# Kernel tuning notes

Hardware: AMD Instinct MI355X
Metric: run time of the kernel (lower is better)

## Reference

```python
import jax, jax.numpy as jnp
import numpy as np

N_PAIRS = 1_600_000   # total neighbor pairs (len(idx_i))
N_ATOMS = 50_000      # number of distinct center atoms (avg 32 neighbors each)


def setup_inputs() -> dict:
    key = jax.random.key(0)
    # sorted center indices -> consecutive ragged segments, like a neighbor list
    idx_i = jnp.sort(jax.random.randint(key, (N_PAIRS,), 0, N_ATOMS, dtype=jnp.int32))
    return {"idx_i": idx_i}


def reference(idx_i):
    # NOTE: output shape is data-dependent (sum_i C(c_i,2)), so this runs eagerly
    # (the concrete sizes below are python ints pulled from the input values),
    # exactly mirroring torch.unique_consecutive + per-segment torch.combinations.
    n = idx_i.shape[0]
    # --- unique_consecutive(return_counts=True), vectorized ---
    change = jnp.concatenate([jnp.ones((1,), bool), idx_i[1:] != idx_i[:-1]])
    seg_id = jnp.cumsum(change.astype(jnp.int32)) - 1          # [n] segment id per pair
    n_seg = int(seg_id[-1]) + 1
    counts = jnp.bincount(seg_id, length=n_seg)                 # [n_seg] c_i
    seg_off = jnp.concatenate([jnp.zeros((1,), counts.dtype), jnp.cumsum(counts)[:-1]])
    # --- per-segment number of unordered pairs C(c,2) ---
    tri_counts = counts * (counts - 1) // 2
    tri_off = jnp.concatenate([jnp.zeros((1,), tri_counts.dtype), jnp.cumsum(tri_counts)[:-1]])
    T = int(jnp.sum(tri_counts))
    # --- one flat vectorized pass over all T triples ---
    idx_i_triples = jnp.repeat(jnp.arange(n_seg, dtype=jnp.int32), tri_counts,
                               total_repeat_length=T)           # [T] segment index
    r = jnp.arange(T, dtype=counts.dtype) - tri_off[idx_i_triples]  # local triple rank
    c = counts[idx_i_triples]                                   # segment size per triple
    M = c * (c - 1) // 2
    rr = M - 1 - r                                              # rank counted from the end
    # triangular-root decode of condensed upper-triangle index (c is small -> fp32 exact)
    a_rev = jnp.floor((jnp.sqrt(8.0 * rr.astype(jnp.float32) + 1.0) - 1.0) / 2.0).astype(c.dtype)
    a = c - 2 - a_rev                                           # first local neighbor pos
    b = c - 1 - (rr - a_rev * (a_rev + 1) // 2)                 # second local neighbor pos (> a)
    base = seg_off[idx_i_triples]
    idx_j_triples = base + a
    idx_k_triples = base + b
    return (idx_i_triples, idx_j_triples, idx_k_triples)
```

## Files before the change

### kernel.cpp

```cpp
#include <hip/hip_runtime.h>

#define THREADS 256
#define EPT 8
#define FILL_BLOCKS 4096

__device__ __forceinline__ int blockReduceSum(int v, int* sdata) {
    int tid = threadIdx.x;
    sdata[tid] = v;
    __syncthreads();
    for (int off = THREADS >> 1; off > 0; off >>= 1) {
        if (tid < off) sdata[tid] += sdata[tid + off];
        __syncthreads();
    }
    int r = sdata[0];
    __syncthreads();
    return r;
}

__device__ __forceinline__ int blockScanIncl(int v, int* sdata) {
    int tid = threadIdx.x;
    sdata[tid] = v;
    __syncthreads();
    for (int off = 1; off < THREADS; off <<= 1) {
        int t = 0;
        if (tid >= off) t = sdata[tid - off];
        __syncthreads();
        if (tid >= off) sdata[tid] += t;
        __syncthreads();
    }
    int r = sdata[tid];
    __syncthreads();
    return r;
}

__device__ __forceinline__ int blockExclScanMax(int v, int* sdata) {
    int tid = threadIdx.x;
    sdata[tid] = v;
    __syncthreads();
    for (int off = 1; off < THREADS; off <<= 1) {
        int t = -1;
        if (tid >= off) t = sdata[tid - off];
        __syncthreads();
        if (tid >= off) sdata[tid] = max(sdata[tid], t);
        __syncthreads();
    }
    int r = (tid == 0) ? -1 : sdata[tid - 1];
    __syncthreads();
    return r;
}

__device__ int findPrevStart(const int* __restrict__ idx, int B0,
                             int* sdata, int* s_found) {
    int tid = threadIdx.x;
    if (tid == 0) *s_found = -1;
    __syncthreads();
    int res = -1;
    for (int step = 0; res < 0; ++step) {
        int p = B0 - 1 - step * THREADS - tid;
        int cand = -1;
        if (p >= 0) {
            bool f = (p == 0) || (idx[p - 1] != idx[p]);
            if (f) cand = p;
        }
        sdata[tid] = cand;
        __syncthreads();
        for (int off = THREADS >> 1; off > 0; off >>= 1) {
            if (tid < off) sdata[tid] = max(sdata[tid], sdata[tid + off]);
            __syncthreads();
        }
        if (tid == 0 && sdata[0] >= 0) *s_found = sdata[0];
        __syncthreads();
        res = *s_found;
        __syncthreads();
    }
    return res;
}

__global__ void k_chunkstats(const int* __restrict__ idx, int n,
                             int* __restrict__ chunkCnt,
                             int* __restrict__ chunkTriSum) {
    __shared__ int sdata[THREADS];
    __shared__ int s_tmp;
    int tid = threadIdx.x, bid = blockIdx.x;
    int B0 = bid * (THREADS * EPT);

    int prevStart = 0;
    if (bid > 0) prevStart = findPrevStart(idx, B0, sdata, &s_tmp);

    int base = B0 + tid * EPT;
    int cnt = 0, myLast = -1;
    for (int j = 0; j < EPT; ++j) {
        int p = base + j;
        if (p < n) {
            bool f = (p == 0) || (idx[p - 1] != idx[p]);
            if (f) { ++cnt; myLast = p; }
        }
    }
    int before = blockExclScanMax(myLast, sdata);
    int lastStart = max(prevStart, before);
    int sumq = 0;
    for (int j = 0; j < EPT; ++j) {
        int p = base + j;
        if (p < n) {
            if ((p == 0) || (idx[p - 1] != idx[p])) lastStart = p;
            sumq += p - lastStart;
        }
    }
    int c = blockReduceSum(cnt, sdata);
    int q = blockReduceSum(sumq, sdata);
    if (tid == 0) { chunkCnt[bid] = c; chunkTriSum[bid] = q; }
}

__global__ void k_emit(const int* __restrict__ idx, int n, int NB,
                       const int* __restrict__ chunkCnt,
                       const int* __restrict__ chunkTriSum,
                       int* __restrict__ segOff, int* __restrict__ triOff,
                       int* __restrict__ nsegPtr) {
    __shared__ int sdata[THREADS];
    __shared__ int s_tmp;
    int tid = threadIdx.x, bid = blockIdx.x;
    int B0 = bid * (THREADS * EPT);

    int prevStart = 0;
    if (bid > 0) prevStart = findPrevStart(idx, B0, sdata, &s_tmp);

    int pv = 0, tv = 0;
    for (int i = tid; i < bid; i += THREADS) {
        pv += chunkCnt[i];
        tv += chunkTriSum[i];
    }
    int segBase = blockReduceSum(pv, sdata);
    int triBase = blockReduceSum(tv, sdata);

    int base = B0 + tid * EPT;
    int cnt = 0, myLast = -1;
    for (int j = 0; j < EPT; ++j) {
        int p = base + j;
        if (p < n) {
            bool f = (p == 0) || (idx[p - 1] != idx[p]);
            if (f) { ++cnt; myLast = p; }
        }
    }
    int before = blockExclScanMax(myLast, sdata);
    int lastStart0 = max(prevStart, before);

    int lastStart = lastStart0;
    int sumq = 0;
    for (int j = 0; j < EPT; ++j) {
        int p = base + j;
        if (p < n) {
            if ((p == 0) || (idx[p - 1] != idx[p])) lastStart = p;
            sumq += p - lastStart;
        }
    }

    int inclC = blockScanIncl(cnt, sdata);
    int inclQ = blockScanIncl(sumq, sdata);
    int ord  = segBase + inclC - cnt;
    int tcur = triBase + inclQ - sumq;

    lastStart = lastStart0;
    for (int j = 0; j < EPT; ++j) {
        int p = base + j;
        if (p < n) {
            bool f = (p == 0) || (idx[p - 1] != idx[p]);
            if (f) {
                segOff[ord] = p;
                triOff[ord] = tcur;
                ++ord;
                lastStart = p;
            }
            tcur += p - lastStart;
        }
    }
    if (bid == NB - 1 && tid == THREADS - 1) {
        int nseg = segBase + inclC;
        *nsegPtr = nseg;
        segOff[nseg] = n;
    }
}

__device__ __forceinline__ void decodeRank(int rr, int c, int& a, int& b) {
    int k = (int)floorf((sqrtf((float)(8 * rr + 1)) - 1.0f) * 0.5f);
    if (k < 0) k = 0;
    while ((k + 1) * (k + 2) / 2 <= rr) ++k;
    while (k * (k + 1) / 2 > rr) --k;
    a = c - 2 - k;
    b = c - 1 - (rr - k * (k + 1) / 2);
}

__device__ __forceinline__ void emitOne(int r, int M, int c, int t0, int baseP,
                                        int s, int* __restrict__ outI,
                                        int* __restrict__ outJ,
                                        int* __restrict__ outK) {
    int a, b;
    decodeRank(M - 1 - r, c, a, b);
    int t = t0 + r;
    outI[t] = s;
    outJ[t] = baseP + a;
    outK[t] = baseP + b;
}

template <int PH>
__device__ __forceinline__ void storeQuad(int* __restrict__ P, int t, int4 v) {
    if constexpr (PH == 0) {
        *reinterpret_cast<int4*>(P + t) = v;
    } else if constexpr (PH == 2) {
        *reinterpret_cast<int2*>(P + t)     = make_int2(v.x, v.y);
        *reinterpret_cast<int2*>(P + t + 2) = make_int2(v.z, v.w);
    } else {
        P[t] = v.x;
        *reinterpret_cast<int2*>(P + t + 1) = make_int2(v.y, v.z);
        P[t + 3] = v.w;
    }
}

template <int TMOD4>
__global__ void k_fill(const int* __restrict__ segOff,
                       const int* __restrict__ triOff,
                       const int* __restrict__ nsegPtr, int T,
                       int* __restrict__ outI, int* __restrict__ outJ,
                       int* __restrict__ outK) {
    constexpr int PHJ = TMOD4 & 3;
    constexpr int PHK = (2 * TMOD4) & 3;
    int nseg = *nsegPtr;
    int w = blockIdx.x * (THREADS / 64) + (threadIdx.x >> 6);
    int lane = threadIdx.x & 63;
    int nW = gridDim.x * (THREADS / 64);
    long long tlo = (long long)T * w / nW;
    long long thi = (long long)T * (w + 1) / nW;
    if (tlo >= thi) return;

    int lo = 0, hi = nseg - 1;
    while (lo < hi) {
        int mid = (lo + hi + 1) >> 1;
        if (triOff[mid] <= (int)tlo) lo = mid; else hi = mid - 1;
    }
    int s = lo;
    long long t = tlo;
    while (t < thi && s < nseg) {
        int baseP = segOff[s];
        int c = segOff[s + 1] - baseP;
        int M = c * (c - 1) / 2;
        int t0 = triOff[s];
        int rstart = (int)(t - t0);
        int rend = M;
        { long long cap = thi - t0; if (cap < (long long)rend) rend = (int)cap; }

        int rA = rstart + ((4 - ((t0 + rstart) & 3)) & 3);
        if (rA > rend) rA = rend;
        int rB = rA + ((rend - rA) & ~3);

        for (int r = rstart + lane; r < rA; r += 64)
            emitOne(r, M, c, t0, baseP, s, outI, outJ, outK);
        for (int r = rB + lane; r < rend; r += 64)
            emitOne(r, M, c, t0, baseP, s, outI, outJ, outK);

        int nq = (rB - rA) >> 2;
        for (int q = lane; q < nq; q += 64) {
            int r = rA + 4 * q;
            int a0, b0;
            decodeRank(M - 1 - r, c, a0, b0);
            int a1 = (b0 == c - 1) ? a0 + 1 : a0;
            int b1 = (b0 == c - 1) ? a0 + 2 : b0 + 1;
            int a2 = (b1 == c - 1) ? a1 + 1 : a1;
            int b2 = (b1 == c - 1) ? a1 + 2 : b1 + 1;
            int a3 = (b2 == c - 1) ? a2 + 1 : a2;
            int b3 = (b2 == c - 1) ? a2 + 2 : b2 + 1;
            int tt = t0 + r;
            storeQuad<0>(outI, tt, make_int4(s, s, s, s));
            storeQuad<PHJ>(outJ, tt,
                make_int4(baseP + a0, baseP + a1, baseP + a2, baseP + a3));
            storeQuad<PHK>(outK, tt,
                make_int4(baseP + b0, baseP + b1, baseP + b2, baseP + b3));
        }
        t = (long long)t0 + rend;
        ++s;
    }
}

extern "C" void kernel_launch(void* const* d_in, const int* in_sizes, int n_in,
                              void* d_out, int out_size, void* d_ws, size_t ws_size,
                              hipStream_t stream) {
    const int* idx = (const int*)d_in[0];
    int n = in_sizes[0];
    int T = out_size / 3;
    int* out = (int*)d_out;
    int* ws = (int*)d_ws;

    int* nsegPtr     = ws;
    int* chunkCnt    = ws + 16;
    int* chunkTriSum = ws + 16 + 8192;
    int* segOff      = ws + 16 + 16384;
    int* triOff      = segOff + (n + 1);

    int chunk = THREADS * EPT;
    int NB = (n + chunk - 1) / chunk;

    hipLaunchKernelGGL(k_chunkstats, dim3(NB), dim3(THREADS), 0, stream,
                       idx, n, chunkCnt, chunkTriSum);
    hipLaunchKernelGGL(k_emit, dim3(NB), dim3(THREADS), 0, stream,
                       idx, n, NB, chunkCnt, chunkTriSum,
                       segOff, triOff, nsegPtr);
    int* outI = out;
    int* outJ = out + T;
    int* outK = out + 2 * T;
    switch (T & 3) {
        case 0:
            hipLaunchKernelGGL((k_fill<0>), dim3(FILL_BLOCKS), dim3(THREADS), 0,
                               stream, segOff, triOff, nsegPtr, T, outI, outJ, outK);
            break;
        case 1:
            hipLaunchKernelGGL((k_fill<1>), dim3(FILL_BLOCKS), dim3(THREADS), 0,
                               stream, segOff, triOff, nsegPtr, T, outI, outJ, outK);
            break;
        case 2:
            hipLaunchKernelGGL((k_fill<2>), dim3(FILL_BLOCKS), dim3(THREADS), 0,
                               stream, segOff, triOff, nsegPtr, T, outI, outJ, outK);
            break;
        default:
            hipLaunchKernelGGL((k_fill<3>), dim3(FILL_BLOCKS), dim3(THREADS), 0,
                               stream, segOff, triOff, nsegPtr, T, outI, outJ, outK);
            break;
    }
}
```

Measured before the change: 82.35 us.

## Split fill into per-output-stream wavefronts writing one array each

```diff
diff --git a/kernel.cpp b/kernel.cpp
--- a/kernel.cpp
+++ b/kernel.cpp
@@ -189,16 +189,12 @@
     b = c - 1 - (rr - k * (k + 1) / 2);
 }
 
-__device__ __forceinline__ void emitOne(int r, int M, int c, int t0, int baseP,
-                                        int s, int* __restrict__ outI,
-                                        int* __restrict__ outJ,
-                                        int* __restrict__ outK) {
+template <int PASS>
+__device__ __forceinline__ int rankValue(int r, int M, int c, int baseP, int s) {
+    if constexpr (PASS == 0) { (void)M; (void)c; (void)baseP; return s; }
     int a, b;
     decodeRank(M - 1 - r, c, a, b);
-    int t = t0 + r;
-    outI[t] = s;
-    outJ[t] = baseP + a;
-    outK[t] = baseP + b;
+    return (PASS == 1) ? baseP + a : baseP + b;
 }
 
 template <int PH>
@@ -215,22 +211,11 @@
     }
 }
 
-template <int TMOD4>
-__global__ void k_fill(const int* __restrict__ segOff,
-                       const int* __restrict__ triOff,
-                       const int* __restrict__ nsegPtr, int T,
-                       int* __restrict__ outI, int* __restrict__ outJ,
-                       int* __restrict__ outK) {
-    constexpr int PHJ = TMOD4 & 3;
-    constexpr int PHK = (2 * TMOD4) & 3;
-    int nseg = *nsegPtr;
-    int w = blockIdx.x * (THREADS / 64) + (threadIdx.x >> 6);
-    int lane = threadIdx.x & 63;
-    int nW = gridDim.x * (THREADS / 64);
-    long long tlo = (long long)T * w / nW;
-    long long thi = (long long)T * (w + 1) / nW;
-    if (tlo >= thi) return;
-
+template <int PASS, int PH>
+__device__ void fillStream(const int* __restrict__ segOff,
+                           const int* __restrict__ triOff,
+                           int nseg, long long tlo, long long thi, int lane,
+                           int* __restrict__ P) {
     int lo = 0, hi = nseg - 1;
     while (lo < hi) {
         int mid = (lo + hi + 1) >> 1;
@@ -252,31 +237,62 @@
         int rB = rA + ((rend - rA) & ~3);
 
         for (int r = rstart + lane; r < rA; r += 64)
-            emitOne(r, M, c, t0, baseP, s, outI, outJ, outK);
+            P[t0 + r] = rankValue<PASS>(r, M, c, baseP, s);
         for (int r = rB + lane; r < rend; r += 64)
-            emitOne(r, M, c, t0, baseP, s, outI, outJ, outK);
+            P[t0 + r] = rankValue<PASS>(r, M, c, baseP, s);
 
         int nq = (rB - rA) >> 2;
         for (int q = lane; q < nq; q += 64) {
             int r = rA + 4 * q;
-            int a0, b0;
-            decodeRank(M - 1 - r, c, a0, b0);
-            int a1 = (b0 == c - 1) ? a0 + 1 : a0;
-            int b1 = (b0 == c - 1) ? a0 + 2 : b0 + 1;
-            int a2 = (b1 == c - 1) ? a1 + 1 : a1;
-            int b2 = (b1 == c - 1) ? a1 + 2 : b1 + 1;
-            int a3 = (b2 == c - 1) ? a2 + 1 : a2;
-            int b3 = (b2 == c - 1) ? a2 + 2 : b2 + 1;
-            int tt = t0 + r;
-            storeQuad<0>(outI, tt, make_int4(s, s, s, s));
-            storeQuad<PHJ>(outJ, tt,
-                make_int4(baseP + a0, baseP + a1, baseP + a2, baseP + a3));
-            storeQuad<PHK>(outK, tt,
-                make_int4(baseP + b0, baseP + b1, baseP + b2, baseP + b3));
+            int4 v;
+            if constexpr (PASS == 0) {
+                v = make_int4(s, s, s, s);
+            } else {
+                int a0, b0;
+                decodeRank(M - 1 - r, c, a0, b0);
+                int a1 = (b0 == c - 1) ? a0 + 1 : a0;
+                int b1 = (b0 == c - 1) ? a0 + 2 : b0 + 1;
+                int a2 = (b1 == c - 1) ? a1 + 1 : a1;
+                int b2 = (b1 == c - 1) ? a1 + 2 : b1 + 1;
+                int a3 = (b2 == c - 1) ? a2 + 1 : a2;
+                int b3 = (b2 == c - 1) ? a2 + 2 : b2 + 1;
+                v = (PASS == 1)
+                    ? make_int4(baseP + a0, baseP + a1, baseP + a2, baseP + a3)
+                    : make_int4(baseP + b0, baseP + b1, baseP + b2, baseP + b3);
+            }
+            storeQuad<PH>(P, t0 + r, v);
         }
         t = (long long)t0 + rend;
         ++s;
     }
+}
+
+template <int TMOD4>
+__global__ void k_fill(const int* __restrict__ segOff,
+                       const int* __restrict__ triOff,
+                       const int* __restrict__ nsegPtr, int T,
+                       int* __restrict__ outI, int* __restrict__ outJ,
+                       int* __restrict__ outK) {
+    constexpr int PHJ = TMOD4 & 3;
+    constexpr int PHK = (2 * TMOD4) & 3;
+    int nseg = *nsegPtr;
+    int gw = blockIdx.x * (THREADS / 64) + (threadIdx.x >> 6);
+    int lane = threadIdx.x & 63;
+    int nW = gridDim.x * (THREADS / 64);
+    int nSW = nW / 3;
+    if (gw >= 3 * nSW) return;
+    int pass = gw / nSW;
+    int sw = gw - pass * nSW;
+    long long tlo = (long long)T * sw / nSW;
+    long long thi = (long long)T * (sw + 1) / nSW;
+    if (tlo >= thi) return;
+
+    if (pass == 0)
+        fillStream<0, 0>(segOff, triOff, nseg, tlo, thi, lane, outI);
+    else if (pass == 1)
+        fillStream<1, PHJ>(segOff, triOff, nseg, tlo, thi, lane, outJ);
+    else
+        fillStream<2, PHK>(segOff, triOff, nseg, tlo, thi, lane, outK);
 }
 
 extern "C" void kernel_launch(void* const* d_in, const int* in_sizes, int n_in,
```

After: 95.20 us. +15.6%, slower.

## Tile fill kernel by segment groups with shared-memory offsets and block-wide quad stores

Applied to the files above, without the earlier changes.

```diff
diff --git a/kernel.cpp b/kernel.cpp
--- a/kernel.cpp
+++ b/kernel.cpp
@@ -2,7 +2,8 @@
 
 #define THREADS 256
 #define EPT 8
-#define FILL_BLOCKS 4096
+#define FILL_BLOCKS 1024
+#define SEGS_PER_TILE 64
 
 __device__ __forceinline__ int blockReduceSum(int v, int* sdata) {
     int tid = threadIdx.x;
@@ -187,18 +188,6 @@
     while (k * (k + 1) / 2 > rr) --k;
     a = c - 2 - k;
     b = c - 1 - (rr - k * (k + 1) / 2);
-}
-
-__device__ __forceinline__ void emitOne(int r, int M, int c, int t0, int baseP,
-                                        int s, int* __restrict__ outI,
-                                        int* __restrict__ outJ,
-                                        int* __restrict__ outK) {
-    int a, b;
-    decodeRank(M - 1 - r, c, a, b);
-    int t = t0 + r;
-    outI[t] = s;
-    outJ[t] = baseP + a;
-    outK[t] = baseP + b;
 }
 
 template <int PH>
@@ -223,59 +212,72 @@
                        int* __restrict__ outK) {
     constexpr int PHJ = TMOD4 & 3;
     constexpr int PHK = (2 * TMOD4) & 3;
+    __shared__ int sSeg[SEGS_PER_TILE + 1];
+    __shared__ int sTri[SEGS_PER_TILE + 1];
     int nseg = *nsegPtr;
-    int w = blockIdx.x * (THREADS / 64) + (threadIdx.x >> 6);
-    int lane = threadIdx.x & 63;
-    int nW = gridDim.x * (THREADS / 64);
-    long long tlo = (long long)T * w / nW;
-    long long thi = (long long)T * (w + 1) / nW;
-    if (tlo >= thi) return;
-
-    int lo = 0, hi = nseg - 1;
-    while (lo < hi) {
-        int mid = (lo + hi + 1) >> 1;
-        if (triOff[mid] <= (int)tlo) lo = mid; else hi = mid - 1;
-    }
-    int s = lo;
-    long long t = tlo;
-    while (t < thi && s < nseg) {
-        int baseP = segOff[s];
-        int c = segOff[s + 1] - baseP;
-        int M = c * (c - 1) / 2;
-        int t0 = triOff[s];
-        int rstart = (int)(t - t0);
-        int rend = M;
-        { long long cap = thi - t0; if (cap < (long long)rend) rend = (int)cap; }
-
-        int rA = rstart + ((4 - ((t0 + rstart) & 3)) & 3);
-        if (rA > rend) rA = rend;
-        int rB = rA + ((rend - rA) & ~3);
-
-        for (int r = rstart + lane; r < rA; r += 64)
-            emitOne(r, M, c, t0, baseP, s, outI, outJ, outK);
-        for (int r = rB + lane; r < rend; r += 64)
-            emitOne(r, M, c, t0, baseP, s, outI, outJ, outK);
-
-        int nq = (rB - rA) >> 2;
-        for (int q = lane; q < nq; q += 64) {
-            int r = rA + 4 * q;
-            int a0, b0;
-            decodeRank(M - 1 - r, c, a0, b0);
-            int a1 = (b0 == c - 1) ? a0 + 1 : a0;
-            int b1 = (b0 == c - 1) ? a0 + 2 : b0 + 1;
-            int a2 = (b1 == c - 1) ? a1 + 1 : a1;
-            int b2 = (b1 == c - 1) ? a1 + 2 : b1 + 1;
-            int a3 = (b2 == c - 1) ? a2 + 1 : a2;
-            int b3 = (b2 == c - 1) ? a2 + 2 : b2 + 1;
-            int tt = t0 + r;
-            storeQuad<0>(outI, tt, make_int4(s, s, s, s));
-            storeQuad<PHJ>(outJ, tt,
-                make_int4(baseP + a0, baseP + a1, baseP + a2, baseP + a3));
-            storeQuad<PHK>(outK, tt,
-                make_int4(baseP + b0, baseP + b1, baseP + b2, baseP + b3));
-        }
-        t = (long long)t0 + rend;
-        ++s;
+    int tid = threadIdx.x;
+    int nTiles = (nseg + SEGS_PER_TILE - 1) / SEGS_PER_TILE;
+
+    for (int tile = blockIdx.x; tile < nTiles; tile += gridDim.x) {
+        int s0 = tile * SEGS_PER_TILE;
+        int ns = min(SEGS_PER_TILE, nseg - s0);
+        __syncthreads();
+        if (tid <= ns) {
+            sSeg[tid] = segOff[s0 + tid];
+            sTri[tid] = (s0 + tid < nseg) ? triOff[s0 + tid] : T;
+        }
+        __syncthreads();
+        int tBeg = sTri[0], tEnd = sTri[ns];
+        if (tBeg >= tEnd) continue;
+
+        int tA = tBeg + ((4 - (tBeg & 3)) & 3); if (tA > tEnd) tA = tEnd;
+        int tB = tA + ((tEnd - tA) & ~3);
+
+        for (int t = tBeg + tid; t < tA; t += THREADS) {
+            int s = 0; while (t >= sTri[s + 1]) ++s;
+            int base = sSeg[s], c = sSeg[s + 1] - base;
+            int a, b; decodeRank(c * (c - 1) / 2 - 1 - (t - sTri[s]), c, a, b);
+            outI[t] = s0 + s; outJ[t] = base + a; outK[t] = base + b;
+        }
+        for (int t = tB + tid; t < tEnd; t += THREADS) {
+            int s = ns - 1; while (sTri[s] > t) --s;
+            int base = sSeg[s], c = sSeg[s + 1] - base;
+            int a, b; decodeRank(c * (c - 1) / 2 - 1 - (t - sTri[s]), c, a, b);
+            outI[t] = s0 + s; outJ[t] = base + a; outK[t] = base + b;
+        }
+
+        int t = tA + 4 * tid;
+        if (t < tB) {
+            int lo = 0, hi = ns - 1;
+            while (lo < hi) {
+                int mid = (lo + hi + 1) >> 1;
+                if (sTri[mid] <= t) lo = mid; else hi = mid - 1;
+            }
+            int s = lo;
+            for (; t < tB; t += 4 * THREADS) {
+                while (t >= sTri[s + 1]) ++s;
+                int base = sSeg[s], c = sSeg[s + 1] - base;
+                int a, b;
+                decodeRank(c * (c - 1) / 2 - 1 - (t - sTri[s]), c, a, b);
+                int iv[4], jv[4], kv[4];
+                iv[0] = s0 + s; jv[0] = base + a; kv[0] = base + b;
+                int ss = s, cc = c, bb = base;
+                for (int u = 1; u < 4; ++u) {
+                    int tu = t + u;
+                    if (tu < sTri[ss + 1]) {
+                        if (b == cc - 1) { ++a; b = a + 1; } else ++b;
+                    } else {
+                        do { ++ss; } while (tu >= sTri[ss + 1]);
+                        bb = sSeg[ss]; cc = sSeg[ss + 1] - bb;
+                        a = 0; b = 1;
+                    }
+                    iv[u] = s0 + ss; jv[u] = bb + a; kv[u] = bb + b;
+                }
+                storeQuad<0>(outI, t, make_int4(iv[0], iv[1], iv[2], iv[3]));
+                storeQuad<PHJ>(outJ, t, make_int4(jv[0], jv[1], jv[2], jv[3]));
+                storeQuad<PHK>(outK, t, make_int4(kv[0], kv[1], kv[2], kv[3]));
+            }
+        }
     }
 }
 
```

Result: slower. 88.39 us (+7.3%).
